# Performance work log

Measured on AMD Instinct MI355X. Metric: run time of the kernel, lower is better.

The kernel has to match this reference:

```python
import jax, jax.numpy as jnp
import numpy as np

# Production-scale dims (see shape_source)
N = 100000      # nodes
E = 1600000     # shortest-path edges
I = 128         # in_channels
O = 128         # out_channels
K = 5           # max_distance
BN_EPS = 1e-5
GIN_EPS = 0.0   # eps=0.0, trainable_eps=False


def setup_inputs() -> dict:
    key = jax.random.key(0)
    ks = jax.random.split(key, 10)
    node_embeddings = jax.random.normal(ks[0], (N, I), dtype=jnp.float32)
    edge_index = jax.random.randint(ks[1], (2, E), 0, N)          # [2, E] row/col
    edge_weights = jax.random.randint(ks[2], (E,), 1, K + 1)      # SP distance in 1..K
    hop_coef = jax.random.normal(ks[3], (K,), dtype=jnp.float32)
    W1 = jax.random.normal(ks[4], (I, O), dtype=jnp.float32) / np.sqrt(I).astype(np.float32)
    b1 = jnp.zeros((O,), jnp.float32)
    gamma1 = jnp.ones((O,), jnp.float32)
    beta1 = jnp.zeros((O,), jnp.float32)
    W2 = jax.random.normal(ks[5], (O, O), dtype=jnp.float32) / np.sqrt(O).astype(np.float32)
    b2 = jnp.zeros((O,), jnp.float32)
    gamma2 = jnp.ones((O,), jnp.float32)
    beta2 = jnp.zeros((O,), jnp.float32)
    return {
        "node_embeddings": node_embeddings,
        "edge_index": edge_index,
        "edge_weights": edge_weights,
        "hop_coef": hop_coef,
        "W1": W1, "b1": b1, "gamma1": gamma1, "beta1": beta1,
        "W2": W2, "b2": b2, "gamma2": gamma2, "beta2": beta2,
    }


def _batch_norm(x, gamma, beta):
    # BatchNorm1d in training mode: batch mean, biased batch variance
    mean = x.mean(axis=0)
    var = x.var(axis=0)
    return gamma * (x - mean) * jax.lax.rsqrt(var + BN_EPS) + beta


def reference(node_embeddings, edge_index, edge_weights, hop_coef,
              W1, b1, gamma1, beta1, W2, b2, gamma2, beta2):
    # Fused form of the per-hop loop: each edge with SP distance d contributes
    # softmax(hop_coef)[d-1] * x[col] to out[row]. Identical math to K separate
    # sparse.mm's weighted by hop_weights and summed.
    hop_w = jax.nn.softmax(hop_coef)                               # [K]
    valid = (edge_weights >= 1) & (edge_weights <= K)
    w_e = jnp.where(valid, hop_w[jnp.clip(edge_weights - 1, 0, K - 1)], 0.0)  # [E]
    row, col = edge_index[0], edge_index[1]
    msgs = w_e[:, None] * node_embeddings[col]                     # [E, I] gather
    agg = jnp.zeros_like(node_embeddings).at[row].add(msgs)        # [N, I] scatter-add
    h = (1.0 + GIN_EPS) * node_embeddings + agg                    # GIN combine
    h = jax.nn.relu(_batch_norm(h @ W1 + b1, gamma1, beta1))
    h = jax.nn.relu(_batch_norm(h @ W2 + b2, gamma2, beta2))
    return h
```

## Files before the change

### kernel.cpp

```cpp
#include <hip/hip_runtime.h>
#include <hip/hip_bf16.h>


#define RCAP 64

typedef __attribute__((ext_vector_type(8))) short short8;
typedef __attribute__((ext_vector_type(4))) float f32x4;

__device__ inline unsigned short f2bf(float v) {
    unsigned int u = __float_as_uint(v);
    return (unsigned short)((u + 0x7fffu + ((u >> 16) & 1u)) >> 16);
}
__device__ inline float bf2f(unsigned int u) { return __uint_as_float(u << 16); }
__device__ inline float bflo(unsigned int u) { return __uint_as_float(u << 16); }
__device__ inline float bfhi(unsigned int u) { return __uint_as_float(u & 0xFFFF0000u); }

__global__ __launch_bounds__(256) void prep_k(
        const float* __restrict__ hc, float* __restrict__ hwp, float* __restrict__ sums,
        const float* __restrict__ W1, const float* __restrict__ W2,
        unsigned short* __restrict__ w1h, unsigned short* __restrict__ w1l,
        unsigned short* __restrict__ w2h, unsigned short* __restrict__ w2l,
        const float4* __restrict__ x4, uint4* __restrict__ xb, int K, long long n8) {
    int b = blockIdx.x, tid = threadIdx.x;
    if (b == 0) {
        sums[tid] = 0.f; sums[tid + 256] = 0.f;
        if (tid == 0) {
            float tmp[8];
            float m = -1e30f;
            for (int k = 0; k < K; ++k) m = fmaxf(m, hc[k]);
            float s = 0.f;
            for (int k = 0; k < K; ++k) { float e = __expf(hc[k] - m); tmp[k] = e; s += e; }
            float inv = 1.f / s;
            for (int k = 0; k < 8; ++k) hwp[k] = 0.f;
            for (int k = 0; k < K; ++k) hwp[k + 1] = tmp[k] * inv;
        }
        return;
    }
    if (b <= 2) {
        const float* W = (b == 2) ? W2 : W1;
        unsigned short* th = (b == 2) ? w2h : w1h;
        unsigned short* tl = (b == 2) ? w2l : w1l;
        for (int i = tid; i < 16384; i += 256) {
            int k = i >> 7, n = i & 127;
            float v = W[k * 128 + n];
            unsigned short hi = f2bf(v);
            th[n * 128 + k] = hi;
            tl[n * 128 + k] = f2bf(v - bf2f(hi));
        }
        return;
    }
    long long g = (long long)(b - 3) * 256 + tid;
    if (g >= n8) return;
    float4 a = x4[g * 2], c = x4[g * 2 + 1];
    union { unsigned short us[8]; uint4 v; } o;
    o.us[0] = f2bf(a.x); o.us[1] = f2bf(a.y); o.us[2] = f2bf(a.z); o.us[3] = f2bf(a.w);
    o.us[4] = f2bf(c.x); o.us[5] = f2bf(c.y); o.us[6] = f2bf(c.z); o.us[7] = f2bf(c.w);
    xb[g] = o.v;
}

__global__ __launch_bounds__(256) void slot_k(const int* __restrict__ rows,
        const int* __restrict__ cols, const int* __restrict__ ew,
        const float* __restrict__ hwp, int* __restrict__ cur,
        int2* __restrict__ staging, int E, int K) {
    int e = blockIdx.x * 256 + threadIdx.x;
    if (e >= E) return;
    int r = rows[e];
    int d = ew[e];
    if (d < 1 || d > K) d = 0;
    float w = hwp[d];
    int s = atomicAdd(&cur[r], 1);
    if (s < RCAP)
        staging[((size_t)r << 6) + s] = make_int2(cols[e], __float_as_int(w));
}

__global__ __launch_bounds__(256) void gather_k(
        const unsigned short* __restrict__ xb, const int2* __restrict__ staging,
        const int* __restrict__ cur, unsigned short* __restrict__ h, int N) {
    int wid = (blockIdx.x * 256 + threadIdx.x) >> 6;
    if (wid >= N) return;
    int lane = threadIdx.x & 63;
    int g4 = lane >> 4, li = lane & 15;
    int deg = __builtin_amdgcn_readfirstlane(cur[wid]);
    deg = min(deg, RCAP);
    const int2* ep = staging + ((size_t)wid << 6);
    const unsigned short* xrow = xb + li * 8;
    float a0 = 0.f, a1 = 0.f, a2 = 0.f, a3 = 0.f;
    float a4 = 0.f, a5 = 0.f, a6 = 0.f, a7 = 0.f;
    if (g4 == 0) {
        uint4 u = *(const uint4*)(xb + (size_t)wid * 128 + li * 8);
        a0 = bflo(u.x); a1 = bfhi(u.x); a2 = bflo(u.y); a3 = bfhi(u.y);
        a4 = bflo(u.z); a5 = bfhi(u.z); a6 = bflo(u.w); a7 = bfhi(u.w);
    }
    int j = 0;
    for (; j + 16 <= deg; j += 16) {
        int2 p0 = ep[j + g4];
        int2 p1 = ep[j + 4 + g4];
        int2 p2 = ep[j + 8 + g4];
        int2 p3 = ep[j + 12 + g4];
        uint4 u0 = *(const uint4*)(xrow + (size_t)p0.x * 128);
        uint4 u1 = *(const uint4*)(xrow + (size_t)p1.x * 128);
        uint4 u2 = *(const uint4*)(xrow + (size_t)p2.x * 128);
        uint4 u3 = *(const uint4*)(xrow + (size_t)p3.x * 128);
        float w0 = __int_as_float(p0.y), w1 = __int_as_float(p1.y);
        float w2 = __int_as_float(p2.y), w3 = __int_as_float(p3.y);
        a0 = fmaf(w0, bflo(u0.x), a0); a1 = fmaf(w0, bfhi(u0.x), a1);
        a2 = fmaf(w0, bflo(u0.y), a2); a3 = fmaf(w0, bfhi(u0.y), a3);
        a4 = fmaf(w0, bflo(u0.z), a4); a5 = fmaf(w0, bfhi(u0.z), a5);
        a6 = fmaf(w0, bflo(u0.w), a6); a7 = fmaf(w0, bfhi(u0.w), a7);
        a0 = fmaf(w1, bflo(u1.x), a0); a1 = fmaf(w1, bfhi(u1.x), a1);
        a2 = fmaf(w1, bflo(u1.y), a2); a3 = fmaf(w1, bfhi(u1.y), a3);
        a4 = fmaf(w1, bflo(u1.z), a4); a5 = fmaf(w1, bfhi(u1.z), a5);
        a6 = fmaf(w1, bflo(u1.w), a6); a7 = fmaf(w1, bfhi(u1.w), a7);
        a0 = fmaf(w2, bflo(u2.x), a0); a1 = fmaf(w2, bfhi(u2.x), a1);
        a2 = fmaf(w2, bflo(u2.y), a2); a3 = fmaf(w2, bfhi(u2.y), a3);
        a4 = fmaf(w2, bflo(u2.z), a4); a5 = fmaf(w2, bfhi(u2.z), a5);
        a6 = fmaf(w2, bflo(u2.w), a6); a7 = fmaf(w2, bfhi(u2.w), a7);
        a0 = fmaf(w3, bflo(u3.x), a0); a1 = fmaf(w3, bfhi(u3.x), a1);
        a2 = fmaf(w3, bflo(u3.y), a2); a3 = fmaf(w3, bfhi(u3.y), a3);
        a4 = fmaf(w3, bflo(u3.z), a4); a5 = fmaf(w3, bfhi(u3.z), a5);
        a6 = fmaf(w3, bflo(u3.w), a6); a7 = fmaf(w3, bfhi(u3.w), a7);
    }
    for (; j + 4 <= deg; j += 4) {
        int2 p = ep[j + g4];
        uint4 u = *(const uint4*)(xrow + (size_t)p.x * 128);
        float w = __int_as_float(p.y);
        a0 = fmaf(w, bflo(u.x), a0); a1 = fmaf(w, bfhi(u.x), a1);
        a2 = fmaf(w, bflo(u.y), a2); a3 = fmaf(w, bfhi(u.y), a3);
        a4 = fmaf(w, bflo(u.z), a4); a5 = fmaf(w, bfhi(u.z), a5);
        a6 = fmaf(w, bflo(u.w), a6); a7 = fmaf(w, bfhi(u.w), a7);
    }
    if (j < deg) {
        int jj = min(j + g4, deg - 1);
        int2 p = ep[jj];
        float w = (j + g4 < deg) ? __int_as_float(p.y) : 0.f;
        uint4 u = *(const uint4*)(xrow + (size_t)p.x * 128);
        a0 = fmaf(w, bflo(u.x), a0); a1 = fmaf(w, bfhi(u.x), a1);
        a2 = fmaf(w, bflo(u.y), a2); a3 = fmaf(w, bfhi(u.y), a3);
        a4 = fmaf(w, bflo(u.z), a4); a5 = fmaf(w, bfhi(u.z), a5);
        a6 = fmaf(w, bflo(u.w), a6); a7 = fmaf(w, bfhi(u.w), a7);
    }
    a0 += __shfl_xor(a0, 16); a1 += __shfl_xor(a1, 16);
    a2 += __shfl_xor(a2, 16); a3 += __shfl_xor(a3, 16);
    a4 += __shfl_xor(a4, 16); a5 += __shfl_xor(a5, 16);
    a6 += __shfl_xor(a6, 16); a7 += __shfl_xor(a7, 16);
    a0 += __shfl_xor(a0, 32); a1 += __shfl_xor(a1, 32);
    a2 += __shfl_xor(a2, 32); a3 += __shfl_xor(a3, 32);
    a4 += __shfl_xor(a4, 32); a5 += __shfl_xor(a5, 32);
    a6 += __shfl_xor(a6, 32); a7 += __shfl_xor(a7, 32);
    if (g4 == 0) {
        uint4 o;
        o.x = (unsigned int)f2bf(a0) | ((unsigned int)f2bf(a1) << 16);
        o.y = (unsigned int)f2bf(a2) | ((unsigned int)f2bf(a3) << 16);
        o.z = (unsigned int)f2bf(a4) | ((unsigned int)f2bf(a5) << 16);
        o.w = (unsigned int)f2bf(a6) | ((unsigned int)f2bf(a7) << 16);
        *(uint4*)(h + (size_t)wid * 128 + li * 8) = o;
    }
}

__global__ __launch_bounds__(256, 4) void gemm_mfma_k(
        const unsigned short* __restrict__ Ain,
        const unsigned short* __restrict__ Bhg, const unsigned short* __restrict__ Blg,
        const float* __restrict__ bias, unsigned short* __restrict__ zout,
        float* __restrict__ sum_out, float* __restrict__ sq_out, int N) {
    __shared__ unsigned short Bs[128 * 136];
    int tid = threadIdx.x;
    int wave = tid >> 6, lane = tid & 63;
    int n16 = lane & 15, q = lane >> 4;
    int rowbase = blockIdx.x * 128 + wave * 32;

    for (int i = tid; i < 2048; i += 256) {
        int n = i >> 4, c = i & 15;
        *(uint4*)&Bs[n * 136 + c * 8] = *(const uint4*)(Bhg + n * 128 + c * 8);
    }

    short8 afr[4][2];
#pragma unroll
    for (int kk = 0; kk < 4; kk++)
#pragma unroll
        for (int mt = 0; mt < 2; mt++) {
            int ar = rowbase + mt * 16 + n16;
            ar = min(ar, N - 1);
            afr[kk][mt] = *(const short8*)(Ain + (size_t)ar * 128 + kk * 32 + q * 8);
        }

    f32x4 acc[2][8];
#pragma unroll
    for (int mt = 0; mt < 2; mt++)
#pragma unroll
        for (int t = 0; t < 8; t++) acc[mt][t] = (f32x4){0.f, 0.f, 0.f, 0.f};

    __syncthreads();
    int ldsb = n16 * 136 + q * 8;
#pragma unroll
    for (int kk = 0; kk < 4; kk++)
#pragma unroll
        for (int t = 0; t < 8; t++) {
            short8 b = *(const short8*)&Bs[t * 16 * 136 + ldsb + kk * 32];
            acc[0][t] = __builtin_amdgcn_mfma_f32_16x16x32_bf16(afr[kk][0], b, acc[0][t], 0, 0, 0);
            acc[1][t] = __builtin_amdgcn_mfma_f32_16x16x32_bf16(afr[kk][1], b, acc[1][t], 0, 0, 0);
        }
    __syncthreads();
    for (int i = tid; i < 2048; i += 256) {
        int n = i >> 4, c = i & 15;
        *(uint4*)&Bs[n * 136 + c * 8] = *(const uint4*)(Blg + n * 128 + c * 8);
    }
    __syncthreads();
#pragma unroll
    for (int kk = 0; kk < 4; kk++)
#pragma unroll
        for (int t = 0; t < 8; t++) {
            short8 b = *(const short8*)&Bs[t * 16 * 136 + ldsb + kk * 32];
            acc[0][t] = __builtin_amdgcn_mfma_f32_16x16x32_bf16(afr[kk][0], b, acc[0][t], 0, 0, 0);
            acc[1][t] = __builtin_amdgcn_mfma_f32_16x16x32_bf16(afr[kk][1], b, acc[1][t], 0, 0, 0);
        }

    float csum[8], csq[8];
#pragma unroll
    for (int t = 0; t < 8; t++) { csum[t] = 0.f; csq[t] = 0.f; }
#pragma unroll
    for (int t = 0; t < 8; t++) {
        int col = n16 + 16 * t;
        float bv = bias[col];
#pragma unroll
        for (int mt = 0; mt < 2; mt++) {
#pragma unroll
            for (int r = 0; r < 4; r++) {
                int row = rowbase + mt * 16 + q * 4 + r;
                if (row < N) {
                    float v = acc[mt][t][r] + bv;
                    zout[(size_t)row * 128 + col] = f2bf(v);
                    csum[t] += v;
                    csq[t] += v * v;
                }
            }
        }
    }
#pragma unroll
    for (int t = 0; t < 8; t++) {
        csum[t] += __shfl_xor(csum[t], 16);
        csum[t] += __shfl_xor(csum[t], 32);
        csq[t] += __shfl_xor(csq[t], 16);
        csq[t] += __shfl_xor(csq[t], 32);
    }
    __syncthreads();
    float* red = (float*)Bs;
    if (q == 0) {
#pragma unroll
        for (int t = 0; t < 8; t++) {
            int col = n16 + 16 * t;
            red[wave * 128 + col] = csum[t];
            red[512 + wave * 128 + col] = csq[t];
        }
    }
    __syncthreads();
    if (tid < 128) {
        float s = 0.f, qq = 0.f;
#pragma unroll
        for (int w = 0; w < 4; w++) {
            s += red[w * 128 + tid];
            qq += red[512 + w * 128 + tid];
        }
        unsafeAtomicAdd(&sum_out[tid], s);
        unsafeAtomicAdd(&sq_out[tid], qq);
    }
}

__global__ __launch_bounds__(256) void bn1_k(const uint4* __restrict__ z,
        const float* __restrict__ sum, const float* __restrict__ sq,
        const float* __restrict__ gamma, const float* __restrict__ beta,
        uint4* __restrict__ out, long long n8, float invN) {
    __shared__ float sc[128], sh[128];
    int tid = threadIdx.x;
    if (tid < 128) {
        float mean = sum[tid] * invN;
        float var = fmaxf(sq[tid] * invN - mean * mean, 0.f);
        float s = gamma[tid] * rsqrtf(var + 1e-5f);
        sc[tid] = s;
        sh[tid] = beta[tid] - mean * s;
    }
    __syncthreads();
    long long g = (long long)blockIdx.x * 256 + tid;
    if (g >= n8) return;
    uint4 u = z[g];
    int cb = (int)((g * 8) & 127);
    float4 s0 = *(const float4*)&sc[cb], s1 = *(const float4*)&sc[cb + 4];
    float4 t0 = *(const float4*)&sh[cb], t1 = *(const float4*)&sh[cb + 4];
    float v0 = fmaxf(fmaf(bflo(u.x), s0.x, t0.x), 0.f);
    float v1 = fmaxf(fmaf(bfhi(u.x), s0.y, t0.y), 0.f);
    float v2 = fmaxf(fmaf(bflo(u.y), s0.z, t0.z), 0.f);
    float v3 = fmaxf(fmaf(bfhi(u.y), s0.w, t0.w), 0.f);
    float v4 = fmaxf(fmaf(bflo(u.z), s1.x, t1.x), 0.f);
    float v5 = fmaxf(fmaf(bfhi(u.z), s1.y, t1.y), 0.f);
    float v6 = fmaxf(fmaf(bflo(u.w), s1.z, t1.z), 0.f);
    float v7 = fmaxf(fmaf(bfhi(u.w), s1.w, t1.w), 0.f);
    uint4 o;
    o.x = (unsigned int)f2bf(v0) | ((unsigned int)f2bf(v1) << 16);
    o.y = (unsigned int)f2bf(v2) | ((unsigned int)f2bf(v3) << 16);
    o.z = (unsigned int)f2bf(v4) | ((unsigned int)f2bf(v5) << 16);
    o.w = (unsigned int)f2bf(v6) | ((unsigned int)f2bf(v7) << 16);
    out[g] = o;
}

__global__ __launch_bounds__(256) void bn2_k(const unsigned short* __restrict__ z2,
        const float* __restrict__ sum2, const float* __restrict__ sq2,
        const float* __restrict__ gamma, const float* __restrict__ beta,
        float* __restrict__ out, long long n8, float invN) {
    __shared__ float sc[128], sh[128];
    int tid = threadIdx.x;
    if (tid < 128) {
        float mean = sum2[tid] * invN;
        float var = fmaxf(sq2[tid] * invN - mean * mean, 0.f);
        float s = gamma[tid] * rsqrtf(var + 1e-5f);
        sc[tid] = s;
        sh[tid] = beta[tid] - mean * s;
    }
    __syncthreads();
    long long g = (long long)blockIdx.x * 256 + tid;
    if (g >= n8) return;
    uint4 u = ((const uint4*)z2)[g];
    int cb = (int)((g * 8) & 127);
    float4 s0 = *(const float4*)&sc[cb], s1 = *(const float4*)&sc[cb + 4];
    float4 t0 = *(const float4*)&sh[cb], t1 = *(const float4*)&sh[cb + 4];
    float4 o0, o1;
    o0.x = fmaxf(fmaf(bflo(u.x), s0.x, t0.x), 0.f);
    o0.y = fmaxf(fmaf(bfhi(u.x), s0.y, t0.y), 0.f);
    o0.z = fmaxf(fmaf(bflo(u.y), s0.z, t0.z), 0.f);
    o0.w = fmaxf(fmaf(bfhi(u.y), s0.w, t0.w), 0.f);
    o1.x = fmaxf(fmaf(bflo(u.z), s1.x, t1.x), 0.f);
    o1.y = fmaxf(fmaf(bfhi(u.z), s1.y, t1.y), 0.f);
    o1.z = fmaxf(fmaf(bflo(u.w), s1.z, t1.z), 0.f);
    o1.w = fmaxf(fmaf(bfhi(u.w), s1.w, t1.w), 0.f);
    ((float4*)out)[g * 2] = o0;
    ((float4*)out)[g * 2 + 1] = o1;
}

extern "C" void kernel_launch(void* const* d_in, const int* in_sizes, int n_in,
                              void* d_out, int out_size, void* d_ws, size_t ws_size,
                              hipStream_t stream) {
    const float* x   = (const float*)d_in[0];
    const int*   ei  = (const int*)d_in[1];
    const int*   ew  = (const int*)d_in[2];
    const float* hc  = (const float*)d_in[3];
    const float* W1  = (const float*)d_in[4];
    const float* b1  = (const float*)d_in[5];
    const float* g1  = (const float*)d_in[6];
    const float* be1 = (const float*)d_in[7];
    const float* W2  = (const float*)d_in[8];
    const float* b2  = (const float*)d_in[9];
    const float* g2  = (const float*)d_in[10];
    const float* be2 = (const float*)d_in[11];

    int N = in_sizes[0] / 128;
    int E = in_sizes[2];
    int K = in_sizes[3];
    int NE = (E + 255) / 256;
    size_t NF = (size_t)N * 128;
    long long n8 = (long long)(NF / 8);
    int NX = (int)((n8 + 255) / 256);

    unsigned short* h = (unsigned short*)d_ws;
    unsigned short* xb = h + NF;
    unsigned short* z1 = xb;
    unsigned short* a1 = h;
    unsigned short* z2 = xb;
    int2* staging = (int2*)(xb + NF);
    int* cur = (int*)(staging + (size_t)N * RCAP);
    unsigned short* w1h = (unsigned short*)(cur + N);
    unsigned short* w1l = w1h + 16384;
    unsigned short* w2h = w1l + 16384;
    unsigned short* w2l = w2h + 16384;
    float* hwp = (float*)(w2l + 16384);
    float* sums = hwp + 8;
    float* sum1 = sums, *sq1 = sums + 128, *sum2 = sums + 256, *sq2 = sums + 384;

    float invN = 1.0f / (float)N;

    hipMemsetAsync(cur, 0, (size_t)N * sizeof(int), stream);

    prep_k<<<3 + NX, 256, 0, stream>>>(hc, hwp, sums, W1, W2,
        w1h, w1l, w2h, w2l, (const float4*)x, (uint4*)xb, K, n8);
    slot_k<<<NE, 256, 0, stream>>>(ei, ei + E, ew, hwp, cur, staging, E, K);
    {
        long long tot = (long long)N * 64;
        gather_k<<<(int)((tot + 255) / 256), 256, 0, stream>>>(xb, staging, cur, h, N);
    }
    int gblocks = (N + 127) / 128;
    gemm_mfma_k<<<gblocks, 256, 0, stream>>>(h, w1h, w1l, b1, z1, sum1, sq1, N);
    bn1_k<<<NX, 256, 0, stream>>>((const uint4*)z1, sum1, sq1, g1, be1,
        (uint4*)a1, n8, invN);
    gemm_mfma_k<<<gblocks, 256, 0, stream>>>(a1, w2h, w2l, b2, z2, sum2, sq2, N);
    bn2_k<<<NX, 256, 0, stream>>>(z2, sum2, sq2, g2, be2, (float*)d_out, n8, invN);
}
```

Measured before the change: 465.6 us.

## Pre-bucket edges by destination row range before slotting into staging

Replaces the single random-scatter slot kernel with a count/scan/scatter partition that groups edges into 1024-row buckets, packed into 32-bit words, and then a slotting pass that works on one bucket at a time. This aims to localize the atomics on the per-row counters and the writes into the staging buffer, improving cache locality over fully random rows. It adds three extra kernel launches, a serial single-block scan, and an extra pass over E edges. The new path is guarded by size limits on N, K and workspace.

```diff
diff --git a/kernel.cpp b/kernel.cpp
--- a/kernel.cpp
+++ b/kernel.cpp
@@ -3,6 +3,8 @@
 
 
 #define RCAP 64
+#define P2B 256
+#define BPB 4
 
 typedef __attribute__((ext_vector_type(8))) short short8;
 typedef __attribute__((ext_vector_type(4))) float f32x4;
@@ -56,6 +58,90 @@
     o.us[0] = f2bf(a.x); o.us[1] = f2bf(a.y); o.us[2] = f2bf(a.z); o.us[3] = f2bf(a.w);
     o.us[4] = f2bf(c.x); o.us[5] = f2bf(c.y); o.us[6] = f2bf(c.z); o.us[7] = f2bf(c.w);
     xb[g] = o.v;
+}
+
+__global__ __launch_bounds__(256) void count_k(const int* __restrict__ rows,
+        int* __restrict__ C, int E, int per, int nbukp) {
+    __shared__ int hist[128];
+    int blk = blockIdx.x, tid = threadIdx.x;
+    for (int i = tid; i < nbukp; i += 256) hist[i] = 0;
+    __syncthreads();
+    int e0 = blk * per, e1 = min(E, e0 + per);
+    for (int e = e0 + tid; e < e1; e += 256)
+        atomicAdd(&hist[rows[e] >> 10], 1);
+    __syncthreads();
+    for (int i = tid; i < nbukp; i += 256) C[blk * nbukp + i] = hist[i];
+}
+
+__global__ __launch_bounds__(256) void scan_k(int* __restrict__ C,
+        int* __restrict__ bstart, int nbukp, int nblk) {
+    __shared__ int tot[129];
+    int tid = threadIdx.x;
+    if (tid < nbukp) {
+        int s = 0;
+        for (int b = 0; b < nblk; b++) s += C[b * nbukp + tid];
+        tot[tid] = s;
+    }
+    __syncthreads();
+    if (tid == 0) {
+        int run = 0;
+        for (int b = 0; b < nbukp; b++) {
+            int t = tot[b];
+            tot[b] = run;
+            bstart[b] = run;
+            run += t;
+        }
+        bstart[nbukp] = run;
+    }
+    __syncthreads();
+    if (tid < nbukp) {
+        int run = tot[tid];
+        for (int b = 0; b < nblk; b++) {
+            int c = C[b * nbukp + tid];
+            C[b * nbukp + tid] = run;
+            run += c;
+        }
+    }
+}
+
+__global__ __launch_bounds__(256) void scatter_k(const int* __restrict__ rows,
+        const int* __restrict__ cols, const int* __restrict__ ew,
+        const int* __restrict__ O, unsigned* __restrict__ bucketed,
+        int E, int per, int nbukp, int K) {
+    __shared__ unsigned curs[128];
+    int blk = blockIdx.x, tid = threadIdx.x;
+    for (int i = tid; i < nbukp; i += 256) curs[i] = (unsigned)O[blk * nbukp + i];
+    __syncthreads();
+    int e0 = blk * per, e1 = min(E, e0 + per);
+    for (int e = e0 + tid; e < e1; e += 256) {
+        int r = rows[e];
+        int c = cols[e];
+        int d = ew[e];
+        if (d < 1 || d > K) d = 0;
+        unsigned idx = atomicAdd(&curs[r >> 10], 1u);
+        bucketed[idx] = (unsigned)d | ((unsigned)c << 3) | ((unsigned)(r & 1023) << 20);
+    }
+}
+
+__global__ __launch_bounds__(256) void slot3_k(const unsigned* __restrict__ bucketed,
+        const int* __restrict__ bstart, const float* __restrict__ hwp,
+        int* __restrict__ cur, int2* __restrict__ staging, int nbukp) {
+    int bucket = blockIdx.x % nbukp, sub = blockIdx.x / nbukp;
+    int s0 = bstart[bucket], s1 = bstart[bucket + 1];
+    int cnt = s1 - s0;
+    int qlo = s0 + (int)((long long)cnt * sub / BPB);
+    int qhi = s0 + (int)((long long)cnt * (sub + 1) / BPB);
+    int rbase = bucket << 10;
+    for (int e = qlo + threadIdx.x; e < qhi; e += 256) {
+        unsigned u = bucketed[e];
+        int d = u & 7;
+        int col = (u >> 3) & 0x1FFFF;
+        int row = rbase + (int)(u >> 20);
+        float w = hwp[d];
+        int s = atomicAdd(&cur[row], 1);
+        if (s < RCAP)
+            staging[((size_t)row << 6) + s] = make_int2(col, __float_as_int(w));
+    }
 }
 
 __global__ __launch_bounds__(256) void slot_k(const int* __restrict__ rows,
@@ -353,7 +439,6 @@
     int N = in_sizes[0] / 128;
     int E = in_sizes[2];
     int K = in_sizes[3];
-    int NE = (E + 255) / 256;
     size_t NF = (size_t)N * 128;
     long long n8 = (long long)(NF / 8);
     int NX = (int)((n8 + 255) / 256);
@@ -372,6 +457,14 @@
     float* hwp = (float*)(w2l + 16384);
     float* sums = hwp + 8;
     float* sum1 = sums, *sq1 = sums + 128, *sum2 = sums + 256, *sq2 = sums + 384;
+    int nbuk  = (N + 1023) >> 10;
+    int nbukp = (nbuk + 7) & ~7;
+    int* C = (int*)(sums + 512);
+    int* bstart = C + (size_t)P2B * nbukp;
+    unsigned* bucketed = (unsigned*)(bstart + nbukp + 1);
+    size_t ws_need = (size_t)((char*)(bucketed + E) - (char*)d_ws);
+    bool use_bucketed = (nbukp <= 128) && (N <= (1 << 17)) && (K <= 7)
+                        && (ws_need <= ws_size);
 
     float invN = 1.0f / (float)N;
 
@@ -379,7 +472,15 @@
 
     prep_k<<<3 + NX, 256, 0, stream>>>(hc, hwp, sums, W1, W2,
         w1h, w1l, w2h, w2l, (const float4*)x, (uint4*)xb, K, n8);
-    slot_k<<<NE, 256, 0, stream>>>(ei, ei + E, ew, hwp, cur, staging, E, K);
+    if (use_bucketed) {
+        int per = (E + P2B - 1) / P2B;
+        count_k<<<P2B, 256, 0, stream>>>(ei, C, E, per, nbukp);
+        scan_k<<<1, 256, 0, stream>>>(C, bstart, nbukp, P2B);
+        scatter_k<<<P2B, 256, 0, stream>>>(ei, ei + E, ew, C, bucketed, E, per, nbukp, K);
+        slot3_k<<<nbukp * BPB, 256, 0, stream>>>(bucketed, bstart, hwp, cur, staging, nbukp);
+    } else {
+        slot_k<<<(E + 255) / 256, 256, 0, stream>>>(ei, ei + E, ew, hwp, cur, staging, E, K);
+    }
     {
         long long tot = (long long)N * 64;
         gather_k<<<(int)((tot + 255) / 256), 256, 0, stream>>>(xb, staging, cur, h, N);
```

New measurement: 524.0 us. 1.13x slower.
